# Performance work log

Measured on AMD Instinct MI355X. Metric: run time of the kernel, lower is better.

## Reference

```python
import jax, jax.numpy as jnp
import numpy as np

B, C, H, W = 2, 256, 64, 64
NUM_HEADS = 4
HEAD_DIM = C // NUM_HEADS
N = H * W


def setup_inputs() -> dict:
    key = jax.random.key(0)
    ks = jax.random.split(key, 10)
    x = jax.random.normal(ks[0], (B, C, H, W), dtype=jnp.float32)
    # mostly-True mask; diagonal forced True so every row has a valid key
    m = jax.random.uniform(ks[1], (B, N, N)) > 0.1
    spatial_mask = m | jnp.eye(N, dtype=bool)[None]
    s = 1.0 / np.sqrt(C)
    wq = jax.random.normal(ks[2], (C, C), dtype=jnp.float32) * s
    bq = jnp.zeros((C,), jnp.float32)
    wk = jax.random.normal(ks[3], (C, C), dtype=jnp.float32) * s
    bk = jnp.zeros((C,), jnp.float32)
    wv = jax.random.normal(ks[4], (C, C), dtype=jnp.float32) * s
    bv = jnp.zeros((C,), jnp.float32)
    # torch zero-inits out_proj; use random weights for a non-trivial baseline
    wo = jax.random.normal(ks[5], (C, C), dtype=jnp.float32) * s
    bo = jnp.zeros((C,), jnp.float32)
    return {"x": x, "spatial_mask": spatial_mask, "wq": wq, "bq": bq,
            "wk": wk, "bk": bk, "wv": wv, "bv": bv, "wo": wo, "bo": bo}


def reference(x, spatial_mask, wq, bq, wk, bk, wv, bv, wo, bo):
    b, c, h, w = x.shape
    n = h * w
    nh, hd = NUM_HEADS, HEAD_DIM
    scale = hd ** -0.5
    x_flat = x.reshape(b, c, n).transpose(0, 2, 1)           # [b, n, c]
    q = (x_flat @ wq.T + bq).reshape(b, n, nh, hd).transpose(0, 2, 1, 3)
    k = (x_flat @ wk.T + bk).reshape(b, n, nh, hd).transpose(0, 2, 1, 3)
    v = (x_flat @ wv.T + bv).reshape(b, n, nh, hd).transpose(0, 2, 1, 3)
    logits = jnp.einsum('bhqd,bhkd->bhqk', q, k) * scale      # [b, nh, n, n]
    logits = jnp.where(spatial_mask[:, None], logits, -jnp.inf)
    attn = jax.nn.softmax(logits, axis=-1)                    # dropout = identity (eval)
    out = jnp.einsum('bhqk,bhkd->bhqd', attn, v)              # [b, nh, n, hd]
    out = out.transpose(0, 2, 1, 3).reshape(b, n, c)
    out = out @ wo.T + bo
    return out.transpose(0, 2, 1).reshape(b, c, h, w)
```

## Files before the change

### kernel.cpp

```cpp
#include <hip/hip_runtime.h>
#include <math.h>

namespace {
constexpr int B_    = 2;
constexpr int C_    = 256;
constexpr int NHEAD = 4;
constexpr int HDIM  = 64;
constexpr int NTOK  = 4096;
constexpr float SCALE = 0.125f;
constexpr float LOG2E = 1.44269504f;
}

typedef _Float16 half8  __attribute__((ext_vector_type(8)));
typedef _Float16 half4  __attribute__((ext_vector_type(4)));
typedef float    floatx4 __attribute__((ext_vector_type(4)));

__global__ __launch_bounds__(256) void pack_mask(
    const unsigned int* __restrict__ m32, unsigned int* __restrict__ packed)
{
    int c0 = 0, c1 = 0, c2 = 0, c3 = 0;
    #pragma unroll
    for (int i = 0; i < 16; i++) {
        const unsigned int d = m32[i];
        c0 += (d == 0x00000001u);
        c1 += (d == 0x3F803F80u);
        c2 += (d == 0x3F800000u);
        c3 += (d == 0x01010101u);
    }
    int fmt = 1, best = c1;
    if (c0 > best) { best = c0; fmt = 0; }
    if (c2 > best) { best = c2; fmt = 2; }
    if (c3 > best) { best = c3; fmt = 3; }

    const unsigned int W = blockIdx.x * 256 + threadIdx.x;
    unsigned int bits = 0;
    if (fmt == 1) {
        const uint4* p4 = (const uint4*)(m32 + (size_t)W * 16);
        #pragma unroll
        for (int i = 0; i < 4; i++) {
            const uint4 v = p4[i];
            const unsigned int d[4] = { v.x, v.y, v.z, v.w };
            #pragma unroll
            for (int j = 0; j < 4; j++) {
                const int e = i * 8 + j * 2;
                bits |= ((d[j] & 0xFFFFu) ? 1u : 0u) << e;
                bits |= ((d[j] >> 16)     ? 1u : 0u) << (e + 1);
            }
        }
    } else if (fmt != 3) {
        const uint4* p4 = (const uint4*)(m32 + (size_t)W * 32);
        #pragma unroll
        for (int i = 0; i < 8; i++) {
            const uint4 v = p4[i];
            bits |= (v.x ? 1u : 0u) << (i * 4 + 0);
            bits |= (v.y ? 1u : 0u) << (i * 4 + 1);
            bits |= (v.z ? 1u : 0u) << (i * 4 + 2);
            bits |= (v.w ? 1u : 0u) << (i * 4 + 3);
        }
    } else {
        const uint4* p4 = (const uint4*)(m32 + (size_t)W * 8);
        #pragma unroll
        for (int i = 0; i < 2; i++) {
            const uint4 v = p4[i];
            const unsigned int d[4] = { v.x, v.y, v.z, v.w };
            #pragma unroll
            for (int j = 0; j < 4; j++) {
                const int e = (i * 4 + j) * 4;
                bits |= ((d[j] & 0x000000FFu) ? 1u : 0u) << (e + 0);
                bits |= ((d[j] & 0x0000FF00u) ? 1u : 0u) << (e + 1);
                bits |= ((d[j] & 0x00FF0000u) ? 1u : 0u) << (e + 2);
                bits |= ((d[j] & 0xFF000000u) ? 1u : 0u) << (e + 3);
            }
        }
    }
    packed[W] = bits;
}

__global__ __launch_bounds__(256) void qkv_mfma(
    const float* __restrict__ x,
    const float* __restrict__ wq, const float* __restrict__ bq,
    const float* __restrict__ wk, const float* __restrict__ bk,
    const float* __restrict__ wv, const float* __restrict__ bv,
    _Float16* __restrict__ qo, _Float16* __restrict__ ko,
    _Float16* __restrict__ vo)
{
    const int nt = blockIdx.x;
    const int h  = blockIdx.y;
    const int b  = blockIdx.z / 3;
    const int p  = blockIdx.z % 3;

    const float* w; const float* bias;
    if (p == 0)      { w = wq; bias = bq; }
    else if (p == 1) { w = wk; bias = bk; }
    else             { w = wv; bias = bv; }

    const int t    = threadIdx.x;
    const int wid  = t >> 6;
    const int lane = t & 63;
    const int quad = lane >> 4;
    const int l15  = lane & 15;
    const int n0  = nt * 64;
    const int co0 = h * 64;

    __shared__ _Float16 wsh[64 * 72];
    __shared__ _Float16 xsh[64 * 72];
    __shared__ _Float16 tbuf[64 * 72];

    const int srow = t >> 2;
    const int sc   = (t & 3) * 16;
    const int cr   = t >> 4;
    const int nu   = (t & 15) * 4;

    floatx4 acc[4];
    #pragma unroll
    for (int i = 0; i < 4; i++) acc[i] = (floatx4)0.f;

    const float* xb = x + (size_t)b * C_ * NTOK;

    for (int c0 = 0; c0 < C_; c0 += 64) {
        {
            const float* wr = &w[(size_t)(co0 + srow) * C_ + c0 + sc];
            half8 h0, h1;
            #pragma unroll
            for (int u = 0; u < 2; u++) {
                const float4 a = *(const float4*)&wr[u * 4];
                h0[u*4+0]=(_Float16)a.x; h0[u*4+1]=(_Float16)a.y;
                h0[u*4+2]=(_Float16)a.z; h0[u*4+3]=(_Float16)a.w;
            }
            #pragma unroll
            for (int u = 0; u < 2; u++) {
                const float4 a = *(const float4*)&wr[8 + u * 4];
                h1[u*4+0]=(_Float16)a.x; h1[u*4+1]=(_Float16)a.y;
                h1[u*4+2]=(_Float16)a.z; h1[u*4+3]=(_Float16)a.w;
            }
            *(half8*)&wsh[srow * 72 + sc]     = h0;
            *(half8*)&wsh[srow * 72 + sc + 8] = h1;
        }
        {
            #pragma unroll
            for (int pass = 0; pass < 4; pass++) {
                const int cl = pass * 16 + cr;
                const float4 v = *(const float4*)&xb[(size_t)(c0 + cl) * NTOK + n0 + nu];
                xsh[(nu + 0) * 72 + cl] = (_Float16)v.x;
                xsh[(nu + 1) * 72 + cl] = (_Float16)v.y;
                xsh[(nu + 2) * 72 + cl] = (_Float16)v.z;
                xsh[(nu + 3) * 72 + cl] = (_Float16)v.w;
            }
        }
        __syncthreads();
        const half8 a0 = *(const half8*)&wsh[(wid * 16 + l15) * 72 + quad * 8];
        const half8 a1 = *(const half8*)&wsh[(wid * 16 + l15) * 72 + 32 + quad * 8];
        #pragma unroll
        for (int nt2 = 0; nt2 < 4; nt2++) {
            const half8 b0 = *(const half8*)&xsh[(nt2 * 16 + l15) * 72 + quad * 8];
            const half8 b1 = *(const half8*)&xsh[(nt2 * 16 + l15) * 72 + 32 + quad * 8];
            acc[nt2] = __builtin_amdgcn_mfma_f32_16x16x32_f16(a0, b0, acc[nt2], 0, 0, 0);
            acc[nt2] = __builtin_amdgcn_mfma_f32_16x16x32_f16(a1, b1, acc[nt2], 0, 0, 0);
        }
        __syncthreads();
    }

    const float4 bb4 = *(const float4*)&bias[co0 + wid * 16 + quad * 4];
    const float bb[4] = { bb4.x, bb4.y, bb4.z, bb4.w };

    if (p < 2) {
        const float osc = (p == 0) ? (SCALE * LOG2E) : 1.0f;
        #pragma unroll
        for (int nt2 = 0; nt2 < 4; nt2++) {
            half4 hv;
            #pragma unroll
            for (int i = 0; i < 4; i++)
                hv[i] = (_Float16)((acc[nt2][i] + bb[i]) * osc);
            *(half4*)&tbuf[(nt2 * 16 + l15) * 72 + wid * 16 + quad * 4] = hv;
        }
        __syncthreads();
        _Float16* dh = (p == 0 ? qo : ko) + (size_t)(b * NHEAD + h) * NTOK * HDIM;
        const half8 o0 = *(const half8*)&tbuf[srow * 72 + sc];
        const half8 o1 = *(const half8*)&tbuf[srow * 72 + sc + 8];
        *(half8*)&dh[(size_t)(n0 + srow) * HDIM + sc]     = o0;
        *(half8*)&dh[(size_t)(n0 + srow) * HDIM + sc + 8] = o1;
    } else {
        #pragma unroll
        for (int nt2 = 0; nt2 < 4; nt2++)
            #pragma unroll
            for (int i = 0; i < 4; i++)
                tbuf[(wid * 16 + quad * 4 + i) * 72 + nt2 * 16 + l15] =
                    (_Float16)(acc[nt2][i] + bb[i]);
        __syncthreads();
        _Float16* vth = vo + (size_t)(b * NHEAD + h) * HDIM * NTOK;
        const half8 o0 = *(const half8*)&tbuf[srow * 72 + sc];
        const half8 o1 = *(const half8*)&tbuf[srow * 72 + sc + 8];
        *(half8*)&vth[(size_t)srow * NTOK + n0 + sc]     = o0;
        *(half8*)&vth[(size_t)srow * NTOK + n0 + sc + 8] = o1;
    }
}

__global__ __launch_bounds__(256) void attn(
    const _Float16* __restrict__ q, const _Float16* __restrict__ k,
    const _Float16* __restrict__ vt, const unsigned int* __restrict__ mpacked,
    _Float16* __restrict__ ao)
{
    const int b  = blockIdx.z;
    const int h  = blockIdx.y;
    const int q0 = blockIdx.x * 64;
    const int t    = threadIdx.x;
    const int w    = t >> 6;
    const int lane = t & 63;
    const int quad = lane >> 4;
    const int l15  = lane & 15;

    __shared__ _Float16 ks[2][64 * 72];
    __shared__ _Float16 vs[2][64 * 72];
    __shared__ _Float16 ps[64 * 72];

    const size_t head_off = (size_t)(b * NHEAD + h) * NTOK * HDIM;
    const _Float16* qb  = q  + head_off;
    const _Float16* kb  = k  + head_off;
    const _Float16* vtb = vt + head_off;
    const unsigned int* mrow = mpacked + (size_t)b * NTOK * 128;

    const int qrow = q0 + w * 16 + l15;
    half8 aq0 = *(const half8*)&qb[(size_t)qrow * HDIM + quad * 8];
    half8 aq1 = *(const half8*)&qb[(size_t)qrow * HDIM + 32 + quad * 8];
    const unsigned int* mq = &mrow[(size_t)qrow * 128];

    const int srow = t >> 2;
    const int scol = (t & 3) * 16;

    half8 kreg0 = *(const half8*)&kb[(size_t)srow * HDIM + scol];
    half8 kreg1 = *(const half8*)&kb[(size_t)srow * HDIM + scol + 8];
    half8 vreg0 = *(const half8*)&vtb[(size_t)srow * NTOK + scol];
    half8 vreg1 = *(const half8*)&vtb[(size_t)srow * NTOK + scol + 8];

    float l_loc = 0.f;
    floatx4 o_acc[4];
    #pragma unroll
    for (int i = 0; i < 4; i++) o_acc[i] = (floatx4)0.f;

    for (int kt = 0; kt < NTOK / 64; kt++) {
        const int k0 = kt * 64;
        _Float16* ksc = ks[kt & 1];
        _Float16* vsc = vs[kt & 1];
        *(half8*)&ksc[srow * 72 + scol]     = kreg0;
        *(half8*)&ksc[srow * 72 + scol + 8] = kreg1;
        *(half8*)&vsc[srow * 72 + scol]     = vreg0;
        *(half8*)&vsc[srow * 72 + scol + 8] = vreg1;
        __syncthreads();

        if (kt + 1 < NTOK / 64) {
            kreg0 = *(const half8*)&kb[(size_t)(k0 + 64 + srow) * HDIM + scol];
            kreg1 = *(const half8*)&kb[(size_t)(k0 + 64 + srow) * HDIM + scol + 8];
            vreg0 = *(const half8*)&vtb[(size_t)srow * NTOK + k0 + 64 + scol];
            vreg1 = *(const half8*)&vtb[(size_t)srow * NTOK + k0 + 64 + scol + 8];
        }
        const uint2 mw = *(const uint2*)&mq[k0 >> 5];

        floatx4 sa[4];
        #pragma unroll
        for (int ct = 0; ct < 4; ct++) {
            sa[ct] = (floatx4)0.f;
            const half8 ka0 = *(const half8*)&ksc[(ct * 16 + l15) * 72 + quad * 8];
            const half8 ka1 = *(const half8*)&ksc[(ct * 16 + l15) * 72 + 32 + quad * 8];
            sa[ct] = __builtin_amdgcn_mfma_f32_16x16x32_f16(ka0, aq0, sa[ct], 0, 0, 0);
            sa[ct] = __builtin_amdgcn_mfma_f32_16x16x32_f16(ka1, aq1, sa[ct], 0, 0, 0);
        }

        #pragma unroll
        for (int ct = 0; ct < 4; ct++) {
            const unsigned int word = (ct < 2) ? mw.x : mw.y;
            const unsigned nib = (word >> (((ct & 1) << 4) + quad * 4)) & 0xFu;
            half4 pv;
            #pragma unroll
            for (int i = 0; i < 4; i++) {
                const float v = ((nib >> i) & 1u) ? sa[ct][i] : -3.0e38f;
                const float p = exp2f(fminf(v, 15.f));
                l_loc += p;
                pv[i] = (_Float16)p;
            }
            *(half4*)&ps[(w * 16 + l15) * 72 + ct * 16 + quad * 4] = pv;
        }

        const half8 pb0 = *(const half8*)&ps[(w * 16 + l15) * 72 + quad * 8];
        const half8 pb1 = *(const half8*)&ps[(w * 16 + l15) * 72 + 32 + quad * 8];
        #pragma unroll
        for (int dt = 0; dt < 4; dt++) {
            const half8 va0 = *(const half8*)&vsc[(dt * 16 + l15) * 72 + quad * 8];
            const half8 va1 = *(const half8*)&vsc[(dt * 16 + l15) * 72 + 32 + quad * 8];
            o_acc[dt] = __builtin_amdgcn_mfma_f32_16x16x32_f16(va0, pb0, o_acc[dt], 0, 0, 0);
            o_acc[dt] = __builtin_amdgcn_mfma_f32_16x16x32_f16(va1, pb1, o_acc[dt], 0, 0, 0);
        }
    }

    l_loc += __shfl_xor(l_loc, 16, 64);
    l_loc += __shfl_xor(l_loc, 32, 64);
    const float inv = (l_loc > 0.f) ? (1.0f / l_loc) : 0.f;

    _Float16* aob = ao + ((size_t)b * NTOK + q0 + w * 16 + l15) * C_ + h * 64;
    #pragma unroll
    for (int dt = 0; dt < 4; dt++) {
        half4 r;
        #pragma unroll
        for (int rr = 0; rr < 4; rr++) r[rr] = (_Float16)(o_acc[dt][rr] * inv);
        *(half4*)&aob[dt * 16 + quad * 4] = r;
    }
}

__global__ __launch_bounds__(256) void out_mfma(
    const _Float16* __restrict__ ao, const float* __restrict__ wo,
    const float* __restrict__ bo, float* __restrict__ out)
{
    const int nt  = blockIdx.x;
    const int cot = blockIdx.y;
    const int b   = blockIdx.z;
    const int t    = threadIdx.x;
    const int wid  = t >> 6;
    const int lane = t & 63;
    const int quad = lane >> 4;
    const int l15  = lane & 15;
    const int n0  = nt * 64;
    const int co0 = cot * 64;

    __shared__ _Float16 wsh[64 * 72];
    __shared__ _Float16 ash[64 * 72];
    __shared__ float    tf[64 * 68];

    const int srow = t >> 2;
    const int sc   = (t & 3) * 16;

    floatx4 acc[4];
    #pragma unroll
    for (int i = 0; i < 4; i++) acc[i] = (floatx4)0.f;

    const _Float16* aob = ao + ((size_t)b * NTOK + n0) * C_;

    for (int c0 = 0; c0 < C_; c0 += 64) {
        {
            const float* wr = &wo[(size_t)(co0 + srow) * C_ + c0 + sc];
            half8 h0, h1;
            #pragma unroll
            for (int u = 0; u < 2; u++) {
                const float4 a = *(const float4*)&wr[u * 4];
                h0[u*4+0]=(_Float16)a.x; h0[u*4+1]=(_Float16)a.y;
                h0[u*4+2]=(_Float16)a.z; h0[u*4+3]=(_Float16)a.w;
            }
            #pragma unroll
            for (int u = 0; u < 2; u++) {
                const float4 a = *(const float4*)&wr[8 + u * 4];
                h1[u*4+0]=(_Float16)a.x; h1[u*4+1]=(_Float16)a.y;
                h1[u*4+2]=(_Float16)a.z; h1[u*4+3]=(_Float16)a.w;
            }
            *(half8*)&wsh[srow * 72 + sc]     = h0;
            *(half8*)&wsh[srow * 72 + sc + 8] = h1;
        }
        {
            const _Float16* ar = &aob[(size_t)srow * C_ + c0 + sc];
            *(half8*)&ash[srow * 72 + sc]     = *(const half8*)&ar[0];
            *(half8*)&ash[srow * 72 + sc + 8] = *(const half8*)&ar[8];
        }
        __syncthreads();
        const half8 a0 = *(const half8*)&wsh[(wid * 16 + l15) * 72 + quad * 8];
        const half8 a1 = *(const half8*)&wsh[(wid * 16 + l15) * 72 + 32 + quad * 8];
        #pragma unroll
        for (int nt2 = 0; nt2 < 4; nt2++) {
            const half8 b0 = *(const half8*)&ash[(nt2 * 16 + l15) * 72 + quad * 8];
            const half8 b1 = *(const half8*)&ash[(nt2 * 16 + l15) * 72 + 32 + quad * 8];
            acc[nt2] = __builtin_amdgcn_mfma_f32_16x16x32_f16(a0, b0, acc[nt2], 0, 0, 0);
            acc[nt2] = __builtin_amdgcn_mfma_f32_16x16x32_f16(a1, b1, acc[nt2], 0, 0, 0);
        }
        __syncthreads();
    }

    #pragma unroll
    for (int nt2 = 0; nt2 < 4; nt2++)
        #pragma unroll
        for (int i = 0; i < 4; i++)
            tf[(wid * 16 + quad * 4 + i) * 68 + nt2 * 16 + l15] = acc[nt2][i];
    __syncthreads();

    const int row = t >> 2;
    const int c4  = (t & 3) * 16;
    const float bb = bo[co0 + row];
    float* orow = &out[((size_t)(b * C_ + co0 + row)) * NTOK + n0 + c4];
    #pragma unroll
    for (int u = 0; u < 4; u++) {
        float4 v = *(const float4*)&tf[row * 68 + c4 + u * 4];
        v.x += bb; v.y += bb; v.z += bb; v.w += bb;
        *(float4*)&orow[u * 4] = v;
    }
}

extern "C" void kernel_launch(void* const* d_in, const int* in_sizes, int n_in,
                              void* d_out, int out_size, void* d_ws, size_t ws_size,
                              hipStream_t stream) {
    const float* x    = (const float*)d_in[0];
    const void*  mask = d_in[1];
    const float* wq   = (const float*)d_in[2];
    const float* bq   = (const float*)d_in[3];
    const float* wk   = (const float*)d_in[4];
    const float* bk   = (const float*)d_in[5];
    const float* wv   = (const float*)d_in[6];
    const float* bv   = (const float*)d_in[7];
    const float* wo   = (const float*)d_in[8];
    const float* bo   = (const float*)d_in[9];
    float* out = (float*)d_out;

    const size_t qkv_elems = (size_t)B_ * NHEAD * NTOK * HDIM;
    _Float16* wsh = (_Float16*)d_ws;
    _Float16* qbuf  = wsh;
    _Float16* kbuf  = wsh + qkv_elems;
    _Float16* vtbuf = wsh + 2 * qkv_elems;
    _Float16* aobuf = wsh + 3 * qkv_elems;
    unsigned int* mpacked = (unsigned int*)(wsh + 4 * qkv_elems);

    pack_mask<<<dim3((B_ * NTOK * 128) / 256), 256, 0, stream>>>(
        (const unsigned int*)mask, mpacked);
    qkv_mfma<<<dim3(NTOK / 64, NHEAD, B_ * 3), 256, 0, stream>>>(
        x, wq, bq, wk, bk, wv, bv, qbuf, kbuf, vtbuf);
    attn<<<dim3(NTOK / 64, NHEAD, B_), 256, 0, stream>>>(
        qbuf, kbuf, vtbuf, mpacked, aobuf);
    out_mfma<<<dim3(NTOK / 64, C_ / 64, B_), 256, 0, stream>>>(
        aobuf, wo, bo, out);
}
```

Before: 331.0 us.

## Split attention key range across two warp groups per block with LDS merge

The attention block doubles to 512 threads. Two groups of four waves each process half of the key sequence for the same 64 queries, using separate K/V/P shared buffers. Partial outputs and row sums are then merged through shared memory before normalisation. This raises the number of waves per query tile, aiming to hide latency on a grid of only 512 blocks, but it drops the K/V double buffering in favour of an extra barrier per iteration and adds a final reduction.

```diff
diff --git a/kernel.cpp b/kernel.cpp
--- a/kernel.cpp
+++ b/kernel.cpp
@@ -195,7 +195,7 @@
     }
 }
 
-__global__ __launch_bounds__(256) void attn(
+__global__ __launch_bounds__(512) void attn(
     const _Float16* __restrict__ q, const _Float16* __restrict__ k,
     const _Float16* __restrict__ vt, const unsigned int* __restrict__ mpacked,
     _Float16* __restrict__ ao)
@@ -208,10 +208,20 @@
     const int lane = t & 63;
     const int quad = lane >> 4;
     const int l15  = lane & 15;
-
-    __shared__ _Float16 ks[2][64 * 72];
-    __shared__ _Float16 vs[2][64 * 72];
-    __shared__ _Float16 ps[64 * 72];
+    const int half = w >> 2;
+    const int w4   = w & 3;
+    const int koff = half * (NTOK / 2);
+
+    __shared__ __align__(16) _Float16 ksA[64 * 72];
+    __shared__ __align__(16) _Float16 vsA[64 * 72];
+    __shared__ __align__(16) _Float16 psA[64 * 72];
+    __shared__ __align__(16) _Float16 ksB[64 * 72];
+    __shared__ __align__(16) _Float16 vsB[64 * 72];
+    __shared__ __align__(16) _Float16 psB[64 * 72];
+
+    _Float16* ksc = half ? ksB : ksA;
+    _Float16* vsc = half ? vsB : vsA;
+    _Float16* ps  = half ? psB : psA;
 
     const size_t head_off = (size_t)(b * NHEAD + h) * NTOK * HDIM;
     const _Float16* qb  = q  + head_off;
@@ -219,35 +229,35 @@
     const _Float16* vtb = vt + head_off;
     const unsigned int* mrow = mpacked + (size_t)b * NTOK * 128;
 
-    const int qrow = q0 + w * 16 + l15;
+    const int qrow = q0 + w4 * 16 + l15;
     half8 aq0 = *(const half8*)&qb[(size_t)qrow * HDIM + quad * 8];
     half8 aq1 = *(const half8*)&qb[(size_t)qrow * HDIM + 32 + quad * 8];
     const unsigned int* mq = &mrow[(size_t)qrow * 128];
 
-    const int srow = t >> 2;
-    const int scol = (t & 3) * 16;
-
-    half8 kreg0 = *(const half8*)&kb[(size_t)srow * HDIM + scol];
-    half8 kreg1 = *(const half8*)&kb[(size_t)srow * HDIM + scol + 8];
-    half8 vreg0 = *(const half8*)&vtb[(size_t)srow * NTOK + scol];
-    half8 vreg1 = *(const half8*)&vtb[(size_t)srow * NTOK + scol + 8];
+    const int tl   = t & 255;
+    const int srow = tl >> 2;
+    const int scol = (tl & 3) * 16;
+
+    half8 kreg0 = *(const half8*)&kb[(size_t)(koff + srow) * HDIM + scol];
+    half8 kreg1 = *(const half8*)&kb[(size_t)(koff + srow) * HDIM + scol + 8];
+    half8 vreg0 = *(const half8*)&vtb[(size_t)srow * NTOK + koff + scol];
+    half8 vreg1 = *(const half8*)&vtb[(size_t)srow * NTOK + koff + scol + 8];
 
     float l_loc = 0.f;
     floatx4 o_acc[4];
     #pragma unroll
     for (int i = 0; i < 4; i++) o_acc[i] = (floatx4)0.f;
 
-    for (int kt = 0; kt < NTOK / 64; kt++) {
-        const int k0 = kt * 64;
-        _Float16* ksc = ks[kt & 1];
-        _Float16* vsc = vs[kt & 1];
+    for (int kt = 0; kt < NTOK / 128; kt++) {
+        const int k0 = koff + kt * 64;
+        __syncthreads();
         *(half8*)&ksc[srow * 72 + scol]     = kreg0;
         *(half8*)&ksc[srow * 72 + scol + 8] = kreg1;
         *(half8*)&vsc[srow * 72 + scol]     = vreg0;
         *(half8*)&vsc[srow * 72 + scol + 8] = vreg1;
         __syncthreads();
 
-        if (kt + 1 < NTOK / 64) {
+        if (kt + 1 < NTOK / 128) {
             kreg0 = *(const half8*)&kb[(size_t)(k0 + 64 + srow) * HDIM + scol];
             kreg1 = *(const half8*)&kb[(size_t)(k0 + 64 + srow) * HDIM + scol + 8];
             vreg0 = *(const half8*)&vtb[(size_t)srow * NTOK + k0 + 64 + scol];
@@ -277,11 +287,11 @@
                 l_loc += p;
                 pv[i] = (_Float16)p;
             }
-            *(half4*)&ps[(w * 16 + l15) * 72 + ct * 16 + quad * 4] = pv;
-        }
-
-        const half8 pb0 = *(const half8*)&ps[(w * 16 + l15) * 72 + quad * 8];
-        const half8 pb1 = *(const half8*)&ps[(w * 16 + l15) * 72 + 32 + quad * 8];
+            *(half4*)&ps[(w4 * 16 + l15) * 72 + ct * 16 + quad * 4] = pv;
+        }
+
+        const half8 pb0 = *(const half8*)&ps[(w4 * 16 + l15) * 72 + quad * 8];
+        const half8 pb1 = *(const half8*)&ps[(w4 * 16 + l15) * 72 + 32 + quad * 8];
         #pragma unroll
         for (int dt = 0; dt < 4; dt++) {
             const half8 va0 = *(const half8*)&vsc[(dt * 16 + l15) * 72 + quad * 8];
@@ -293,15 +303,32 @@
 
     l_loc += __shfl_xor(l_loc, 16, 64);
     l_loc += __shfl_xor(l_loc, 32, 64);
-    const float inv = (l_loc > 0.f) ? (1.0f / l_loc) : 0.f;
-
-    _Float16* aob = ao + ((size_t)b * NTOK + q0 + w * 16 + l15) * C_ + h * 64;
-    #pragma unroll
-    for (int dt = 0; dt < 4; dt++) {
-        half4 r;
-        #pragma unroll
-        for (int rr = 0; rr < 4; rr++) r[rr] = (_Float16)(o_acc[dt][rr] * inv);
-        *(half4*)&aob[dt * 16 + quad * 4] = r;
+
+    __syncthreads();
+    float* oex = (float*)ksA;
+    float* lex = (float*)vsA;
+    if (w >= 4) {
+        float* dst = &oex[((size_t)(w - 4) * 64 + lane) * 16];
+        #pragma unroll
+        for (int dt = 0; dt < 4; dt++)
+            *(floatx4*)&dst[dt * 4] = o_acc[dt];
+        if (quad == 0) lex[(w - 4) * 16 + l15] = l_loc;
+    }
+    __syncthreads();
+    if (w < 4) {
+        const float* src = &oex[((size_t)w * 64 + lane) * 16];
+        const float lt = l_loc + lex[w * 16 + l15];
+        const float inv = (lt > 0.f) ? (1.0f / lt) : 0.f;
+        _Float16* aob = ao + ((size_t)b * NTOK + q0 + w * 16 + l15) * C_ + h * 64;
+        #pragma unroll
+        for (int dt = 0; dt < 4; dt++) {
+            const floatx4 o2 = *(const floatx4*)&src[dt * 4];
+            half4 r;
+            #pragma unroll
+            for (int rr = 0; rr < 4; rr++)
+                r[rr] = (_Float16)((o_acc[dt][rr] + o2[rr]) * inv);
+            *(half4*)&aob[dt * 16 + quad * 4] = r;
+        }
     }
 }
 
@@ -416,7 +443,7 @@
         (const unsigned int*)mask, mpacked);
     qkv_mfma<<<dim3(NTOK / 64, NHEAD, B_ * 3), 256, 0, stream>>>(
         x, wq, bq, wk, bk, wv, bv, qbuf, kbuf, vtbuf);
-    attn<<<dim3(NTOK / 64, NHEAD, B_), 256, 0, stream>>>(
+    attn<<<dim3(NTOK / 64, NHEAD, B_), 512, 0, stream>>>(
         qbuf, kbuf, vtbuf, mpacked, aobuf);
     out_mfma<<<dim3(NTOK / 64, C_ / 64, B_), 256, 0, stream>>>(
         aobuf, wo, bo, out);
```

Measured after the change: 318.3 us. 3.9% less time.
